# Performance work log

Measured on AMD Instinct MI355X. Metric: run time of the kernel, lower is better.

The kernel has to match this reference:

```python
import jax, jax.numpy as jnp
import numpy as np

B, N, D_IN, D_B, K = 32, 1024, 1024, 256, 16384


def setup_inputs() -> dict:
    key = jax.random.key(0)
    ks = jax.random.split(key, 8)
    s_in = 1.0 / np.sqrt(D_IN)
    s_b = 1.0 / np.sqrt(D_B)
    return {
        "x": jax.random.normal(ks[0], (B, N, D_IN), dtype=jnp.float32),
        "W_in": jax.random.uniform(ks[1], (D_IN, D_B), jnp.float32, -s_in, s_in),
        "b_in": jax.random.uniform(ks[2], (D_B,), jnp.float32, -s_in, s_in),
        "W_out": jax.random.uniform(ks[3], (D_B, D_IN), jnp.float32, -s_b, s_b),
        "b_out": jax.random.uniform(ks[4], (D_IN,), jnp.float32, -s_b, s_b),
        "codebook": jax.random.normal(ks[5], (K, D_B), dtype=jnp.float32),
        "W_proj": jax.random.uniform(ks[6], (D_B, D_B), jnp.float32, -s_b, s_b),
        "b_proj": jax.random.uniform(ks[7], (D_B,), jnp.float32, -s_b, s_b),
    }


def reference(x, W_in, b_in, W_out, b_out, codebook, W_proj, b_proj):
    # project_in
    z = jnp.einsum('bnd,de->bne', x, W_in) + b_in            # [B,N,Db]
    # SimVQ: projected codebook
    emb = codebook @ W_proj + b_proj                          # [K,Db]
    zf = z.reshape(-1, z.shape[-1])                           # [B*N,Db]
    # squared-distance argmin (cdist pattern)
    d = (jnp.sum(zf**2, axis=1, keepdims=True)
         + jnp.sum(emb**2, axis=1)
         - 2.0 * zf @ emb.T)                                  # [B*N,K]
    q_idx = jnp.argmin(d, axis=1)                             # [B*N]
    quantized = emb[q_idx].reshape(z.shape)                   # [B,N,Db]
    # straight-through
    reg_z = z + jax.lax.stop_gradient(quantized - z)
    # project_out
    x_hat = jnp.einsum('bnd,de->bne', reg_z, W_out) + b_out   # [B,N,Dout]
    bottleneck_rep = q_idx.reshape(z.shape[0], z.shape[1])
    return x_hat, bottleneck_rep, z, emb, reg_z
```

## Files before the change

### kernel.cpp

```cpp
#include <hip/hip_runtime.h>

typedef unsigned int u32;
typedef unsigned long long u64;
typedef unsigned short u16;

#define M_ROWS 32768
#define DB 256
#define DIN 1024
#define KCODES 16384

typedef __attribute__((ext_vector_type(8))) short bf16x8;
typedef __attribute__((ext_vector_type(4))) float f32x4;
typedef __attribute__((ext_vector_type(8))) unsigned short us8;

#define GLOAD16(gp, lp) __builtin_amdgcn_global_load_lds( \
    (const __attribute__((address_space(1))) unsigned int*)(gp), \
    (__attribute__((address_space(3))) unsigned int*)(lp), 16, 0, 0)

__device__ __forceinline__ u32 ford(float f) {
    u32 u = __float_as_uint(f);
    return (u & 0x80000000u) ? ~u : (u | 0x80000000u);
}
__device__ __forceinline__ u64 shfl_xor_u64(u64 v, int m) {
    u32 lo = (u32)v, hi = (u32)(v >> 32);
    lo = (u32)__shfl_xor((int)lo, m, 64);
    hi = (u32)__shfl_xor((int)hi, m, 64);
    return ((u64)hi << 32) | lo;
}
__device__ __forceinline__ u16 f2bf_rne(float f) {
    const u32 u = __float_as_uint(f);
    return (u16)((u + 0x7FFFu + ((u >> 16) & 1u)) >> 16);
}

__global__ __launch_bounds__(256)
void sgemm_f32(const float* __restrict__ A, int lda,
               const float* __restrict__ B, int ldb,
               const float* __restrict__ bias,
               float* __restrict__ C, int ldc, int Kd)
{
    __shared__ float As[16][132];
    __shared__ float Bs[16][132];
    const int t = threadIdx.x;
    const int w = t >> 6, lane = t & 63;
    const int tx = (lane & 7) | ((w & 1) << 3);
    const int ty = ((lane >> 3) & 7) | ((w >> 1) << 3);
    const int rb = blockIdx.x << 7;
    const int cb = blockIdx.y << 7;

    const int sr  = t >> 1;
    const int sk8 = (t & 1) << 3;
    const int bkr = t >> 4;
    const int bc8 = (t & 15) << 3;

    const float* Ap = A + (size_t)(rb + sr) * lda + sk8;
    const float* Bp = B + (size_t)bkr * ldb + cb + bc8;

    float acc[8][8];
#pragma unroll
    for (int i = 0; i < 8; ++i)
#pragma unroll
        for (int j = 0; j < 8; ++j) acc[i][j] = 0.0f;

    float4 a0 = *(const float4*)Ap;
    float4 a1 = *(const float4*)(Ap + 4);
    float4 b0 = *(const float4*)Bp;
    float4 b1 = *(const float4*)(Bp + 4);

    for (int kb = 0; kb < Kd; kb += 16) {
        __syncthreads();
        As[sk8 + 0][sr] = a0.x; As[sk8 + 1][sr] = a0.y;
        As[sk8 + 2][sr] = a0.z; As[sk8 + 3][sr] = a0.w;
        As[sk8 + 4][sr] = a1.x; As[sk8 + 5][sr] = a1.y;
        As[sk8 + 6][sr] = a1.z; As[sk8 + 7][sr] = a1.w;
        *(float4*)&Bs[bkr][bc8]     = b0;
        *(float4*)&Bs[bkr][bc8 + 4] = b1;
        __syncthreads();
        if (kb + 16 < Kd) {
            a0 = *(const float4*)(Ap + kb + 16);
            a1 = *(const float4*)(Ap + kb + 20);
            b0 = *(const float4*)(Bp + (size_t)(kb + 16) * ldb);
            b1 = *(const float4*)(Bp + (size_t)(kb + 16) * ldb + 4);
        }
#pragma unroll
        for (int kk = 0; kk < 16; ++kk) {
            float a[8], b[8];
            *(float4*)&a[0] = *(const float4*)&As[kk][ty * 8];
            *(float4*)&a[4] = *(const float4*)&As[kk][ty * 8 + 4];
            *(float4*)&b[0] = *(const float4*)&Bs[kk][tx * 8];
            *(float4*)&b[4] = *(const float4*)&Bs[kk][tx * 8 + 4];
#pragma unroll
            for (int i = 0; i < 8; ++i)
#pragma unroll
                for (int j = 0; j < 8; ++j)
                    acc[i][j] += a[i] * b[j];
        }
    }

    float bb[8];
#pragma unroll
    for (int j = 0; j < 8; ++j) bb[j] = bias[cb + tx * 8 + j];

#pragma unroll
    for (int i = 0; i < 8; ++i) {
        const size_t off = (size_t)(rb + ty * 8 + i) * ldc + cb + tx * 8;
        *(float4*)&C[off]     = make_float4(acc[i][0] + bb[0], acc[i][1] + bb[1],
                                            acc[i][2] + bb[2], acc[i][3] + bb[3]);
        *(float4*)&C[off + 4] = make_float4(acc[i][4] + bb[4], acc[i][5] + bb[5],
                                            acc[i][6] + bb[6], acc[i][7] + bb[7]);
    }
}

__global__ __launch_bounds__(256)
void split_pack(const float* __restrict__ X, u16* __restrict__ hi,
                u16* __restrict__ lo, float* __restrict__ s2)
{
    const int tid = (blockIdx.x << 8) + threadIdx.x;
    const int row = tid >> 5;
    const int kb  = (tid & 31) << 3;
    const float4 v0 = *(const float4*)(X + ((size_t)row << 8) + kb);
    const float4 v1 = *(const float4*)(X + ((size_t)row << 8) + kb + 4);
    const float f[8] = {v0.x, v0.y, v0.z, v0.w, v1.x, v1.y, v1.z, v1.w};
    us8 hv, lv;
    float s = 0.0f;
#pragma unroll
    for (int e = 0; e < 8; ++e) {
        const u16 h = f2bf_rne(f[e]);
        const float hf = __uint_as_float((u32)h << 16);
        hv[e] = h;
        lv[e] = f2bf_rne(f[e] - hf);
        s += f[e] * f[e];
    }
    const size_t off = ((size_t)(row >> 4) * 8 + (kb >> 5)) * 512
                     + (size_t)((kb >> 3) & 3) * 128 + ((row & 15) << 3);
    *(us8*)(hi + off) = hv;
    *(us8*)(lo + off) = lv;
#pragma unroll
    for (int m = 1; m <= 16; m <<= 1) s += __shfl_xor(s, m, 64);
    if ((threadIdx.x & 31) == 0) s2[row] = s;
}

__global__ __launch_bounds__(256)
void pack_wout(const float* __restrict__ W, u16* __restrict__ hi, u16* __restrict__ lo)
{
    const int tid = (blockIdx.x << 8) + threadIdx.x;
    const int n  = tid >> 5;
    const int kb = (tid & 31) << 3;
    us8 hv, lv;
#pragma unroll
    for (int e = 0; e < 8; ++e) {
        const float f = W[(size_t)(kb + e) * DIN + n];
        const u16 h = f2bf_rne(f);
        hv[e] = h;
        lv[e] = f2bf_rne(f - __uint_as_float((u32)h << 16));
    }
    const size_t off = ((size_t)(n >> 4) * 8 + (kb >> 5)) * 512
                     + (size_t)((kb >> 3) & 3) * 128 + ((n & 15) << 3);
    *(us8*)(hi + off) = hv;
    *(us8*)(lo + off) = lv;
}

__global__ __launch_bounds__(256)
void score_mfma(const u16* __restrict__ zh, const u16* __restrict__ zl,
                const u16* __restrict__ eh, const u16* __restrict__ el,
                const float* __restrict__ e2, u64* __restrict__ partial)
{
    __shared__ u16 smem[4][8][512];
    const int t = threadIdx.x;
    const int w = t >> 6, lane = t & 63;
    const int wr = w >> 1, wc = w & 1;
    const int rb = blockIdx.x << 7, cb = blockIdx.y << 7;
    const u32 lane8 = (u32)lane << 3;
    const int g = lane >> 4, li = lane & 15;

    const u32 zc0 = (u32)((rb >> 4) + w)     * 4096 + lane8;
    const u32 zc1 = (u32)((rb >> 4) + 4 + w) * 4096 + lane8;
    const u32 ec0 = (u32)((cb >> 4) + w)     * 4096 + lane8;
    const u32 ec1 = (u32)((cb >> 4) + 4 + w) * 4096 + lane8;

    u16* ZhL0 = &smem[0][w][0];      u16* ZhL1 = &smem[0][4 + w][0];
    u16* ZlL0 = &smem[1][w][0];      u16* ZlL1 = &smem[1][4 + w][0];
    u16* EhL0 = &smem[2][w][0];      u16* EhL1 = &smem[2][4 + w][0];
    u16* ElL0 = &smem[3][w][0];      u16* ElL1 = &smem[3][4 + w][0];

    int codes[4];
    float e2v[4];
#pragma unroll
    for (int j = 0; j < 4; ++j) {
        codes[j] = cb + wc * 64 + j * 16 + li;
        e2v[j] = e2[codes[j]];
    }

    f32x4 acc[4][4];
#pragma unroll
    for (int i = 0; i < 4; ++i)
#pragma unroll
        for (int j = 0; j < 4; ++j) {
            const float v = -0.5f * e2v[j];
            acc[i][j] = (f32x4){v, v, v, v};
        }

    for (int ks = 0; ks < 8; ++ks) {
        const u32 ko = (u32)ks << 9;
        if (ks) __syncthreads();
        GLOAD16(zh + zc0 + ko, ZhL0);  GLOAD16(zh + zc1 + ko, ZhL1);
        GLOAD16(zl + zc0 + ko, ZlL0);  GLOAD16(zl + zc1 + ko, ZlL1);
        GLOAD16(eh + ec0 + ko, EhL0);  GLOAD16(eh + ec1 + ko, EhL1);
        GLOAD16(el + ec0 + ko, ElL0);  GLOAD16(el + ec1 + ko, ElL1);
        __syncthreads();

        bf16x8 ah[4], al[4], bh[4], bl[4];
#pragma unroll
        for (int i = 0; i < 4; ++i) {
            ah[i] = *(const bf16x8*)&smem[0][wr * 4 + i][lane8];
            al[i] = *(const bf16x8*)&smem[1][wr * 4 + i][lane8];
            bh[i] = *(const bf16x8*)&smem[2][wc * 4 + i][lane8];
            bl[i] = *(const bf16x8*)&smem[3][wc * 4 + i][lane8];
        }
#pragma unroll
        for (int i = 0; i < 4; ++i)
#pragma unroll
            for (int j = 0; j < 4; ++j) {
                acc[i][j] = __builtin_amdgcn_mfma_f32_16x16x32_bf16(ah[i], bh[j], acc[i][j], 0, 0, 0);
                acc[i][j] = __builtin_amdgcn_mfma_f32_16x16x32_bf16(ah[i], bl[j], acc[i][j], 0, 0, 0);
                acc[i][j] = __builtin_amdgcn_mfma_f32_16x16x32_bf16(al[i], bh[j], acc[i][j], 0, 0, 0);
            }
    }

    const int slot = (blockIdx.y << 1) + wc;

#pragma unroll
    for (int i = 0; i < 4; ++i) {
#pragma unroll
        for (int r = 0; r < 4; ++r) {
            const int row = rb + wr * 64 + i * 16 + g * 4 + r;
            const float s0 = acc[i][0][r], s1 = acc[i][1][r];
            const float s2s = acc[i][2][r], s3 = acc[i][3][r];
            const float mm = fmaxf(fmaxf(s0, s1), fmaxf(s2s, s3));
            const u32 cj = (mm == s0) ? (u32)codes[0]
                         : (mm == s1) ? (u32)codes[1]
                         : (mm == s2s) ? (u32)codes[2] : (u32)codes[3];
            u64 key = ((u64)ford(-mm) << 32) | cj;
#pragma unroll
            for (int m = 1; m <= 8; m <<= 1) {
                const u64 o = shfl_xor_u64(key, m);
                key = (o < key) ? o : key;
            }
            if (li == 0) partial[((size_t)row << 8) + slot] = key;
        }
    }
}

__global__ __launch_bounds__(256)
void finalize2(const u64* __restrict__ partial, const float* __restrict__ Z,
               const float* __restrict__ E, const float* __restrict__ z2,
               const float* __restrict__ e2,
               float* __restrict__ bneck, float* __restrict__ regz,
               int* __restrict__ qidx)
{
    const int t = threadIdx.x;
    const int row = (blockIdx.x << 2) + (t >> 6);
    const int lane = t & 63;
    const u64* p = partial + ((size_t)row << 8);

    u64 a1 = ~0ull, a2 = ~0ull;
#pragma unroll
    for (int q = 0; q < 4; ++q) {
        const u64 k = p[(q << 6) + lane];
        if (k < a1) { a2 = a1; a1 = k; }
        else if (k < a2) { a2 = k; }
    }
#pragma unroll
    for (int m = 1; m <= 32; m <<= 1) {
        const u64 b1 = shfl_xor_u64(a1, m);
        const u64 b2 = shfl_xor_u64(a2, m);
        if (b1 < a1) { a2 = (a1 < b2) ? a1 : b2; a1 = b1; }
        else         { a2 = (a2 < b1) ? a2 : b1; }
    }
    const u32 i1 = (u32)a1 & (KCODES - 1);
    const u32 i2 = (u32)a2 & (KCODES - 1);

    const float4 zv  = *(const float4*)(Z + ((size_t)row << 8) + (lane << 2));
    const float4 c1v = *(const float4*)(E + ((size_t)i1 << 8) + (lane << 2));
    const float4 c2v = *(const float4*)(E + ((size_t)i2 << 8) + (lane << 2));
    float s1 = zv.x * c1v.x + zv.y * c1v.y + zv.z * c1v.z + zv.w * c1v.w;
    float s2 = zv.x * c2v.x + zv.y * c2v.y + zv.z * c2v.z + zv.w * c2v.w;
#pragma unroll
    for (int m = 32; m >= 1; m >>= 1) {
        s1 += __shfl_xor(s1, m, 64);
        s2 += __shfl_xor(s2, m, 64);
    }
    const float zz = z2[row];
    const float d1 = (zz + e2[i1]) - 2.0f * s1;
    const float d2 = (zz + e2[i2]) - 2.0f * s2;
    u32 win = i1;
    if (d2 < d1 || (d2 == d1 && i2 < i1)) win = i2;

    if (lane == 0) { qidx[row] = (int)win; bneck[row] = (float)win; }
    const float4 vw = *(const float4*)(E + ((size_t)win << 8) + (lane << 2));
    *(float4*)(regz + ((size_t)row << 8) + (lane << 2)) = vw;
}

__global__ __launch_bounds__(256)
void embout_mfma(const u16* __restrict__ ah_p, const u16* __restrict__ al_p,
                 const u16* __restrict__ bh_p, const u16* __restrict__ bl_p,
                 const float* __restrict__ bias, float* __restrict__ C)
{
    __shared__ u16 smem[4][8][512];
    const int t = threadIdx.x;
    const int w = t >> 6, lane = t & 63;
    const int wr = w >> 1, wc = w & 1;
    const int rb = blockIdx.x << 7, cb = blockIdx.y << 7;
    const u32 lane8 = (u32)lane << 3;
    const int g = lane >> 4, li = lane & 15;

    const u32 ac0 = (u32)((rb >> 4) + w)     * 4096 + lane8;
    const u32 ac1 = (u32)((rb >> 4) + 4 + w) * 4096 + lane8;
    const u32 bc0 = (u32)((cb >> 4) + w)     * 4096 + lane8;
    const u32 bc1 = (u32)((cb >> 4) + 4 + w) * 4096 + lane8;

    u16* AhL0 = &smem[0][w][0];      u16* AhL1 = &smem[0][4 + w][0];
    u16* AlL0 = &smem[1][w][0];      u16* AlL1 = &smem[1][4 + w][0];
    u16* BhL0 = &smem[2][w][0];      u16* BhL1 = &smem[2][4 + w][0];
    u16* BlL0 = &smem[3][w][0];      u16* BlL1 = &smem[3][4 + w][0];

    f32x4 acc[4][4];
#pragma unroll
    for (int i = 0; i < 4; ++i)
#pragma unroll
        for (int j = 0; j < 4; ++j) acc[i][j] = (f32x4){0.f, 0.f, 0.f, 0.f};

    for (int ks = 0; ks < 8; ++ks) {
        const u32 ko = (u32)ks << 9;
        if (ks) __syncthreads();
        GLOAD16(ah_p + ac0 + ko, AhL0);  GLOAD16(ah_p + ac1 + ko, AhL1);
        GLOAD16(al_p + ac0 + ko, AlL0);  GLOAD16(al_p + ac1 + ko, AlL1);
        GLOAD16(bh_p + bc0 + ko, BhL0);  GLOAD16(bh_p + bc1 + ko, BhL1);
        GLOAD16(bl_p + bc0 + ko, BlL0);  GLOAD16(bl_p + bc1 + ko, BlL1);
        __syncthreads();

        bf16x8 ah[4], al[4], bh[4], bl[4];
#pragma unroll
        for (int i = 0; i < 4; ++i) {
            ah[i] = *(const bf16x8*)&smem[0][wr * 4 + i][lane8];
            al[i] = *(const bf16x8*)&smem[1][wr * 4 + i][lane8];
            bh[i] = *(const bf16x8*)&smem[2][wc * 4 + i][lane8];
            bl[i] = *(const bf16x8*)&smem[3][wc * 4 + i][lane8];
        }
#pragma unroll
        for (int i = 0; i < 4; ++i)
#pragma unroll
            for (int j = 0; j < 4; ++j) {
                acc[i][j] = __builtin_amdgcn_mfma_f32_16x16x32_bf16(ah[i], bh[j], acc[i][j], 0, 0, 0);
                acc[i][j] = __builtin_amdgcn_mfma_f32_16x16x32_bf16(ah[i], bl[j], acc[i][j], 0, 0, 0);
                acc[i][j] = __builtin_amdgcn_mfma_f32_16x16x32_bf16(al[i], bh[j], acc[i][j], 0, 0, 0);
            }
    }

    float bv[4];
#pragma unroll
    for (int j = 0; j < 4; ++j) bv[j] = bias[cb + wc * 64 + j * 16 + li];

#pragma unroll
    for (int i = 0; i < 4; ++i)
#pragma unroll
        for (int j = 0; j < 4; ++j) {
            const int col = cb + wc * 64 + j * 16 + li;
#pragma unroll
            for (int r = 0; r < 4; ++r) {
                const int m = rb + wr * 64 + i * 16 + g * 4 + r;
                C[(size_t)m * DIN + col] = acc[i][j][r] + bv[j];
            }
        }
}

__global__ __launch_bounds__(256)
void gather_rows(const int* __restrict__ qidx, const float* __restrict__ S,
                 float* __restrict__ D)
{
    const int row = blockIdx.x;
    const int q = qidx[row] & (KCODES - 1);
    const float4 v = *(const float4*)(S + ((size_t)q << 10) + (threadIdx.x << 2));
    *(float4*)(D + ((size_t)row << 10) + (threadIdx.x << 2)) = v;
}

__global__ __launch_bounds__(256)
void xhat_gemm(const int* __restrict__ qidx, const float* __restrict__ E,
               const float* __restrict__ B, const float* __restrict__ bias,
               float* __restrict__ C)
{
    __shared__ float As[16][132];
    __shared__ float Bs[16][132];
    const int t = threadIdx.x;
    const int w = t >> 6, lane = t & 63;
    const int tx = (lane & 7) | ((w & 1) << 3);
    const int ty = ((lane >> 3) & 7) | ((w >> 1) << 3);
    const int rb = blockIdx.x << 7;
    const int cb = blockIdx.y << 7;

    const int sr  = t >> 1;
    const int sk8 = (t & 1) << 3;
    const int bkr = t >> 4;
    const int bc8 = (t & 15) << 3;

    const int aidx = qidx[rb + sr] & (KCODES - 1);
    const float* Ap = E + (size_t)aidx * DB + sk8;
    const float* Bp = B + (size_t)bkr * DIN + cb + bc8;

    float acc[8][8];
#pragma unroll
    for (int i = 0; i < 8; ++i)
#pragma unroll
        for (int j = 0; j < 8; ++j) acc[i][j] = 0.0f;

    float4 a0 = *(const float4*)Ap;
    float4 a1 = *(const float4*)(Ap + 4);
    float4 b0 = *(const float4*)Bp;
    float4 b1 = *(const float4*)(Bp + 4);

    for (int kb = 0; kb < DB; kb += 16) {
        __syncthreads();
        As[sk8 + 0][sr] = a0.x; As[sk8 + 1][sr] = a0.y;
        As[sk8 + 2][sr] = a0.z; As[sk8 + 3][sr] = a0.w;
        As[sk8 + 4][sr] = a1.x; As[sk8 + 5][sr] = a1.y;
        As[sk8 + 6][sr] = a1.z; As[sk8 + 7][sr] = a1.w;
        *(float4*)&Bs[bkr][bc8]     = b0;
        *(float4*)&Bs[bkr][bc8 + 4] = b1;
        __syncthreads();
        if (kb + 16 < DB) {
            a0 = *(const float4*)(Ap + kb + 16);
            a1 = *(const float4*)(Ap + kb + 20);
            b0 = *(const float4*)(Bp + (size_t)(kb + 16) * DIN);
            b1 = *(const float4*)(Bp + (size_t)(kb + 16) * DIN + 4);
        }
#pragma unroll
        for (int kk = 0; kk < 16; ++kk) {
            float a[8], b[8];
            *(float4*)&a[0] = *(const float4*)&As[kk][ty * 8];
            *(float4*)&a[4] = *(const float4*)&As[kk][ty * 8 + 4];
            *(float4*)&b[0] = *(const float4*)&Bs[kk][tx * 8];
            *(float4*)&b[4] = *(const float4*)&Bs[kk][tx * 8 + 4];
#pragma unroll
            for (int i = 0; i < 8; ++i)
#pragma unroll
                for (int j = 0; j < 8; ++j)
                    acc[i][j] += a[i] * b[j];
        }
    }

    float bb[8];
#pragma unroll
    for (int j = 0; j < 8; ++j) bb[j] = bias[cb + tx * 8 + j];

#pragma unroll
    for (int i = 0; i < 8; ++i) {
        const size_t off = (size_t)(rb + ty * 8 + i) * DIN + cb + tx * 8;
        *(float4*)&C[off]     = make_float4(acc[i][0] + bb[0], acc[i][1] + bb[1],
                                            acc[i][2] + bb[2], acc[i][3] + bb[3]);
        *(float4*)&C[off + 4] = make_float4(acc[i][4] + bb[4], acc[i][5] + bb[5],
                                            acc[i][6] + bb[6], acc[i][7] + bb[7]);
    }
}

extern "C" void kernel_launch(void* const* d_in, const int* in_sizes, int n_in,
                              void* d_out, int out_size, void* d_ws, size_t ws_size,
                              hipStream_t stream)
{
    const float* x        = (const float*)d_in[0];
    const float* W_in     = (const float*)d_in[1];
    const float* b_in     = (const float*)d_in[2];
    const float* W_out    = (const float*)d_in[3];
    const float* b_out    = (const float*)d_in[4];
    const float* codebook = (const float*)d_in[5];
    const float* W_proj   = (const float*)d_in[6];
    const float* b_proj   = (const float*)d_in[7];

    float* out   = (float*)d_out;
    float* xhat  = out;
    float* bneck = out + 33554432;
    float* z     = out + 33587200;
    float* emb   = out + 41975808;
    float* regz  = out + 46170112;

    char* outc = (char*)d_out;
    u64* partial = (u64*)outc;
    u16* eh = (u16*)(outc + 67108864);
    u16* el = (u16*)(outc + 75497472);
    u16* zh = (u16*)(outc + 184680448);
    u16* zl = (u16*)(outc + 201457664);

    char* ws = (char*)d_ws;
    float* e2   = (float*)ws;
    float* z2   = (float*)(ws + 65536);
    int*   qidx = (int*)  (ws + 196608);
    u16*   whh     = (u16*)  (ws + 327680);
    u16*   whl     = (u16*)  (ws + 851968);
    float* emb_out = (float*)(ws + 1376256);
    const bool fast_xhat = (ws_size >= (size_t)1376256 + 67108864);

    sgemm_f32<<<dim3(128, 2), 256, 0, stream>>>(codebook, DB, W_proj, DB, b_proj,
                                                emb, DB, DB);
    split_pack<<<KCODES / 8, 256, 0, stream>>>(emb, eh, el, e2);
    if (fast_xhat) {
        pack_wout<<<DIN / 8, 256, 0, stream>>>(W_out, whh, whl);
        embout_mfma<<<dim3(KCODES / 128, DIN / 128), 256, 0, stream>>>(
            eh, el, whh, whl, b_out, emb_out);
    }
    sgemm_f32<<<dim3(256, 2), 256, 0, stream>>>(x, DIN, W_in, DB, b_in,
                                                z, DB, DIN);
    split_pack<<<M_ROWS / 8, 256, 0, stream>>>(z, zh, zl, z2);
    score_mfma<<<dim3(M_ROWS / 128, KCODES / 128), 256, 0, stream>>>(
        zh, zl, eh, el, e2, partial);
    finalize2<<<M_ROWS / 4, 256, 0, stream>>>(partial, z, emb, z2, e2,
                                              bneck, regz, qidx);
    if (fast_xhat) {
        gather_rows<<<M_ROWS, 256, 0, stream>>>(qidx, emb_out, xhat);
    } else {
        xhat_gemm<<<dim3(256, 8), 256, 0, stream>>>(qidx, emb, W_out, b_out, xhat);
    }
}
```

Measured before the change: 1.411 ms.

## Double-buffer LDS tiles in score and output-projection MFMA kernels

```diff
diff --git a/kernel.cpp b/kernel.cpp
--- a/kernel.cpp
+++ b/kernel.cpp
@@ -164,7 +164,7 @@
                 const u16* __restrict__ eh, const u16* __restrict__ el,
                 const float* __restrict__ e2, u64* __restrict__ partial)
 {
-    __shared__ u16 smem[4][8][512];
+    __shared__ u16 smem[2][4][8][512];
     const int t = threadIdx.x;
     const int w = t >> 6, lane = t & 63;
     const int wr = w >> 1, wc = w & 1;
@@ -177,11 +177,6 @@
     const u32 ec0 = (u32)((cb >> 4) + w)     * 4096 + lane8;
     const u32 ec1 = (u32)((cb >> 4) + 4 + w) * 4096 + lane8;
 
-    u16* ZhL0 = &smem[0][w][0];      u16* ZhL1 = &smem[0][4 + w][0];
-    u16* ZlL0 = &smem[1][w][0];      u16* ZlL1 = &smem[1][4 + w][0];
-    u16* EhL0 = &smem[2][w][0];      u16* EhL1 = &smem[2][4 + w][0];
-    u16* ElL0 = &smem[3][w][0];      u16* ElL1 = &smem[3][4 + w][0];
-
     int codes[4];
     float e2v[4];
 #pragma unroll
@@ -199,22 +194,30 @@
             acc[i][j] = (f32x4){v, v, v, v};
         }
 
+    GLOAD16(zh + zc0, &smem[0][0][w][0]);  GLOAD16(zh + zc1, &smem[0][0][4 + w][0]);
+    GLOAD16(zl + zc0, &smem[0][1][w][0]);  GLOAD16(zl + zc1, &smem[0][1][4 + w][0]);
+    GLOAD16(eh + ec0, &smem[0][2][w][0]);  GLOAD16(eh + ec1, &smem[0][2][4 + w][0]);
+    GLOAD16(el + ec0, &smem[0][3][w][0]);  GLOAD16(el + ec1, &smem[0][3][4 + w][0]);
+
+    int b = 0;
     for (int ks = 0; ks < 8; ++ks) {
-        const u32 ko = (u32)ks << 9;
-        if (ks) __syncthreads();
-        GLOAD16(zh + zc0 + ko, ZhL0);  GLOAD16(zh + zc1 + ko, ZhL1);
-        GLOAD16(zl + zc0 + ko, ZlL0);  GLOAD16(zl + zc1 + ko, ZlL1);
-        GLOAD16(eh + ec0 + ko, EhL0);  GLOAD16(eh + ec1 + ko, EhL1);
-        GLOAD16(el + ec0 + ko, ElL0);  GLOAD16(el + ec1 + ko, ElL1);
         __syncthreads();
+        if (ks < 7) {
+            const u32 ko = (u32)(ks + 1) << 9;
+            const int nb = b ^ 1;
+            GLOAD16(zh + zc0 + ko, &smem[nb][0][w][0]);  GLOAD16(zh + zc1 + ko, &smem[nb][0][4 + w][0]);
+            GLOAD16(zl + zc0 + ko, &smem[nb][1][w][0]);  GLOAD16(zl + zc1 + ko, &smem[nb][1][4 + w][0]);
+            GLOAD16(eh + ec0 + ko, &smem[nb][2][w][0]);  GLOAD16(eh + ec1 + ko, &smem[nb][2][4 + w][0]);
+            GLOAD16(el + ec0 + ko, &smem[nb][3][w][0]);  GLOAD16(el + ec1 + ko, &smem[nb][3][4 + w][0]);
+        }
 
         bf16x8 ah[4], al[4], bh[4], bl[4];
 #pragma unroll
         for (int i = 0; i < 4; ++i) {
-            ah[i] = *(const bf16x8*)&smem[0][wr * 4 + i][lane8];
-            al[i] = *(const bf16x8*)&smem[1][wr * 4 + i][lane8];
-            bh[i] = *(const bf16x8*)&smem[2][wc * 4 + i][lane8];
-            bl[i] = *(const bf16x8*)&smem[3][wc * 4 + i][lane8];
+            ah[i] = *(const bf16x8*)&smem[b][0][wr * 4 + i][lane8];
+            al[i] = *(const bf16x8*)&smem[b][1][wr * 4 + i][lane8];
+            bh[i] = *(const bf16x8*)&smem[b][2][wc * 4 + i][lane8];
+            bl[i] = *(const bf16x8*)&smem[b][3][wc * 4 + i][lane8];
         }
 #pragma unroll
         for (int i = 0; i < 4; ++i)
@@ -224,6 +227,7 @@
                 acc[i][j] = __builtin_amdgcn_mfma_f32_16x16x32_bf16(ah[i], bl[j], acc[i][j], 0, 0, 0);
                 acc[i][j] = __builtin_amdgcn_mfma_f32_16x16x32_bf16(al[i], bh[j], acc[i][j], 0, 0, 0);
             }
+        b ^= 1;
     }
 
     const int slot = (blockIdx.y << 1) + wc;
@@ -305,7 +309,7 @@
                  const u16* __restrict__ bh_p, const u16* __restrict__ bl_p,
                  const float* __restrict__ bias, float* __restrict__ C)
 {
-    __shared__ u16 smem[4][8][512];
+    __shared__ u16 smem[2][4][8][512];
     const int t = threadIdx.x;
     const int w = t >> 6, lane = t & 63;
     const int wr = w >> 1, wc = w & 1;
@@ -318,33 +322,36 @@
     const u32 bc0 = (u32)((cb >> 4) + w)     * 4096 + lane8;
     const u32 bc1 = (u32)((cb >> 4) + 4 + w) * 4096 + lane8;
 
-    u16* AhL0 = &smem[0][w][0];      u16* AhL1 = &smem[0][4 + w][0];
-    u16* AlL0 = &smem[1][w][0];      u16* AlL1 = &smem[1][4 + w][0];
-    u16* BhL0 = &smem[2][w][0];      u16* BhL1 = &smem[2][4 + w][0];
-    u16* BlL0 = &smem[3][w][0];      u16* BlL1 = &smem[3][4 + w][0];
-
     f32x4 acc[4][4];
 #pragma unroll
     for (int i = 0; i < 4; ++i)
 #pragma unroll
         for (int j = 0; j < 4; ++j) acc[i][j] = (f32x4){0.f, 0.f, 0.f, 0.f};
 
+    GLOAD16(ah_p + ac0, &smem[0][0][w][0]);  GLOAD16(ah_p + ac1, &smem[0][0][4 + w][0]);
+    GLOAD16(al_p + ac0, &smem[0][1][w][0]);  GLOAD16(al_p + ac1, &smem[0][1][4 + w][0]);
+    GLOAD16(bh_p + bc0, &smem[0][2][w][0]);  GLOAD16(bh_p + bc1, &smem[0][2][4 + w][0]);
+    GLOAD16(bl_p + bc0, &smem[0][3][w][0]);  GLOAD16(bl_p + bc1, &smem[0][3][4 + w][0]);
+
+    int b = 0;
     for (int ks = 0; ks < 8; ++ks) {
-        const u32 ko = (u32)ks << 9;
-        if (ks) __syncthreads();
-        GLOAD16(ah_p + ac0 + ko, AhL0);  GLOAD16(ah_p + ac1 + ko, AhL1);
-        GLOAD16(al_p + ac0 + ko, AlL0);  GLOAD16(al_p + ac1 + ko, AlL1);
-        GLOAD16(bh_p + bc0 + ko, BhL0);  GLOAD16(bh_p + bc1 + ko, BhL1);
-        GLOAD16(bl_p + bc0 + ko, BlL0);  GLOAD16(bl_p + bc1 + ko, BlL1);
         __syncthreads();
+        if (ks < 7) {
+            const u32 ko = (u32)(ks + 1) << 9;
+            const int nb = b ^ 1;
+            GLOAD16(ah_p + ac0 + ko, &smem[nb][0][w][0]);  GLOAD16(ah_p + ac1 + ko, &smem[nb][0][4 + w][0]);
+            GLOAD16(al_p + ac0 + ko, &smem[nb][1][w][0]);  GLOAD16(al_p + ac1 + ko, &smem[nb][1][4 + w][0]);
+            GLOAD16(bh_p + bc0 + ko, &smem[nb][2][w][0]);  GLOAD16(bh_p + bc1 + ko, &smem[nb][2][4 + w][0]);
+            GLOAD16(bl_p + bc0 + ko, &smem[nb][3][w][0]);  GLOAD16(bl_p + bc1 + ko, &smem[nb][3][4 + w][0]);
+        }
 
         bf16x8 ah[4], al[4], bh[4], bl[4];
 #pragma unroll
         for (int i = 0; i < 4; ++i) {
-            ah[i] = *(const bf16x8*)&smem[0][wr * 4 + i][lane8];
-            al[i] = *(const bf16x8*)&smem[1][wr * 4 + i][lane8];
-            bh[i] = *(const bf16x8*)&smem[2][wc * 4 + i][lane8];
-            bl[i] = *(const bf16x8*)&smem[3][wc * 4 + i][lane8];
+            ah[i] = *(const bf16x8*)&smem[b][0][wr * 4 + i][lane8];
+            al[i] = *(const bf16x8*)&smem[b][1][wr * 4 + i][lane8];
+            bh[i] = *(const bf16x8*)&smem[b][2][wc * 4 + i][lane8];
+            bl[i] = *(const bf16x8*)&smem[b][3][wc * 4 + i][lane8];
         }
 #pragma unroll
         for (int i = 0; i < 4; ++i)
@@ -354,6 +361,7 @@
                 acc[i][j] = __builtin_amdgcn_mfma_f32_16x16x32_bf16(ah[i], bl[j], acc[i][j], 0, 0, 0);
                 acc[i][j] = __builtin_amdgcn_mfma_f32_16x16x32_bf16(al[i], bh[j], acc[i][j], 0, 0, 0);
             }
+        b ^= 1;
     }
 
     float bv[4];
```

Result: slower. 1.469 ms (+4.1%).

## Double-buffer LDS tiles in score kernel to overlap loads with MFMA

Applied to the files above, without the earlier changes.

```diff
diff --git a/kernel.cpp b/kernel.cpp
--- a/kernel.cpp
+++ b/kernel.cpp
@@ -164,7 +164,7 @@
                 const u16* __restrict__ eh, const u16* __restrict__ el,
                 const float* __restrict__ e2, u64* __restrict__ partial)
 {
-    __shared__ u16 smem[4][8][512];
+    __shared__ u16 smem[2][4][8][512];
     const int t = threadIdx.x;
     const int w = t >> 6, lane = t & 63;
     const int wr = w >> 1, wc = w & 1;
@@ -177,11 +177,6 @@
     const u32 ec0 = (u32)((cb >> 4) + w)     * 4096 + lane8;
     const u32 ec1 = (u32)((cb >> 4) + 4 + w) * 4096 + lane8;
 
-    u16* ZhL0 = &smem[0][w][0];      u16* ZhL1 = &smem[0][4 + w][0];
-    u16* ZlL0 = &smem[1][w][0];      u16* ZlL1 = &smem[1][4 + w][0];
-    u16* EhL0 = &smem[2][w][0];      u16* EhL1 = &smem[2][4 + w][0];
-    u16* ElL0 = &smem[3][w][0];      u16* ElL1 = &smem[3][4 + w][0];
-
     int codes[4];
     float e2v[4];
 #pragma unroll
@@ -199,22 +194,36 @@
             acc[i][j] = (f32x4){v, v, v, v};
         }
 
+#define STAGE(B, KO) do { \
+    GLOAD16(zh + zc0 + (KO), &smem[B][0][w][0]);  GLOAD16(zh + zc1 + (KO), &smem[B][0][4 + w][0]); \
+    GLOAD16(zl + zc0 + (KO), &smem[B][1][w][0]);  GLOAD16(zl + zc1 + (KO), &smem[B][1][4 + w][0]); \
+    GLOAD16(eh + ec0 + (KO), &smem[B][2][w][0]);  GLOAD16(eh + ec1 + (KO), &smem[B][2][4 + w][0]); \
+    GLOAD16(el + ec0 + (KO), &smem[B][3][w][0]);  GLOAD16(el + ec1 + (KO), &smem[B][3][4 + w][0]); \
+} while (0)
+
+    asm volatile("s_waitcnt vmcnt(0)" ::: "memory");
+    __builtin_amdgcn_sched_barrier(0);
+
+    STAGE(0, 0u);
+    STAGE(1, 512u);
+
+#pragma unroll
     for (int ks = 0; ks < 8; ++ks) {
-        const u32 ko = (u32)ks << 9;
-        if (ks) __syncthreads();
-        GLOAD16(zh + zc0 + ko, ZhL0);  GLOAD16(zh + zc1 + ko, ZhL1);
-        GLOAD16(zl + zc0 + ko, ZlL0);  GLOAD16(zl + zc1 + ko, ZlL1);
-        GLOAD16(eh + ec0 + ko, EhL0);  GLOAD16(eh + ec1 + ko, EhL1);
-        GLOAD16(el + ec0 + ko, ElL0);  GLOAD16(el + ec1 + ko, ElL1);
-        __syncthreads();
-
+        if (ks < 7) { asm volatile("s_waitcnt vmcnt(8)" ::: "memory"); }
+        else        { asm volatile("s_waitcnt vmcnt(0)" ::: "memory"); }
+        __builtin_amdgcn_sched_barrier(0);
+        __builtin_amdgcn_s_barrier();
+        asm volatile("" ::: "memory");
+        __builtin_amdgcn_sched_barrier(0);
+
+        const int b = ks & 1;
         bf16x8 ah[4], al[4], bh[4], bl[4];
 #pragma unroll
         for (int i = 0; i < 4; ++i) {
-            ah[i] = *(const bf16x8*)&smem[0][wr * 4 + i][lane8];
-            al[i] = *(const bf16x8*)&smem[1][wr * 4 + i][lane8];
-            bh[i] = *(const bf16x8*)&smem[2][wc * 4 + i][lane8];
-            bl[i] = *(const bf16x8*)&smem[3][wc * 4 + i][lane8];
+            ah[i] = *(const bf16x8*)&smem[b][0][wr * 4 + i][lane8];
+            al[i] = *(const bf16x8*)&smem[b][1][wr * 4 + i][lane8];
+            bh[i] = *(const bf16x8*)&smem[b][2][wc * 4 + i][lane8];
+            bl[i] = *(const bf16x8*)&smem[b][3][wc * 4 + i][lane8];
         }
 #pragma unroll
         for (int i = 0; i < 4; ++i)
@@ -224,7 +233,15 @@
                 acc[i][j] = __builtin_amdgcn_mfma_f32_16x16x32_bf16(ah[i], bl[j], acc[i][j], 0, 0, 0);
                 acc[i][j] = __builtin_amdgcn_mfma_f32_16x16x32_bf16(al[i], bh[j], acc[i][j], 0, 0, 0);
             }
-    }
+
+        __builtin_amdgcn_sched_barrier(0);
+        asm volatile("" ::: "memory");
+        __builtin_amdgcn_s_barrier();
+        asm volatile("" ::: "memory");
+        __builtin_amdgcn_sched_barrier(0);
+        if (ks < 6) STAGE(b, (u32)(ks + 2) << 9);
+    }
+#undef STAGE
 
     const int slot = (blockIdx.y << 1) + wc;
 
```

New measurement: 1.433 ms. No clear change (+1.6%).

## Fuse z projection with bf16 hi/lo packing and pre-reduce score partials in-block

Applied to the files above, without the earlier changes.

```diff
diff --git a/kernel.cpp b/kernel.cpp
--- a/kernel.cpp
+++ b/kernel.cpp
@@ -111,6 +111,109 @@
 }
 
 __global__ __launch_bounds__(256)
+void sgemm_z_pack(const float* __restrict__ A, const float* __restrict__ B,
+                  const float* __restrict__ bias, float* __restrict__ C,
+                  u16* __restrict__ zh, u16* __restrict__ zl)
+{
+    __shared__ float As[16][132];
+    __shared__ float Bs[16][132];
+    const int t = threadIdx.x;
+    const int w = t >> 6, lane = t & 63;
+    const int tx = (lane & 7) | ((w & 1) << 3);
+    const int ty = ((lane >> 3) & 7) | ((w >> 1) << 3);
+    const int rb = blockIdx.x << 7;
+    const int cb = blockIdx.y << 7;
+
+    const int sr  = t >> 1;
+    const int sk8 = (t & 1) << 3;
+    const int bkr = t >> 4;
+    const int bc8 = (t & 15) << 3;
+
+    const float* Ap = A + (size_t)(rb + sr) * DIN + sk8;
+    const float* Bp = B + (size_t)bkr * DB + cb + bc8;
+
+    float acc[8][8];
+#pragma unroll
+    for (int i = 0; i < 8; ++i)
+#pragma unroll
+        for (int j = 0; j < 8; ++j) acc[i][j] = 0.0f;
+
+    float4 a0 = *(const float4*)Ap;
+    float4 a1 = *(const float4*)(Ap + 4);
+    float4 b0 = *(const float4*)Bp;
+    float4 b1 = *(const float4*)(Bp + 4);
+
+    for (int kb = 0; kb < DIN; kb += 16) {
+        __syncthreads();
+        As[sk8 + 0][sr] = a0.x; As[sk8 + 1][sr] = a0.y;
+        As[sk8 + 2][sr] = a0.z; As[sk8 + 3][sr] = a0.w;
+        As[sk8 + 4][sr] = a1.x; As[sk8 + 5][sr] = a1.y;
+        As[sk8 + 6][sr] = a1.z; As[sk8 + 7][sr] = a1.w;
+        *(float4*)&Bs[bkr][bc8]     = b0;
+        *(float4*)&Bs[bkr][bc8 + 4] = b1;
+        __syncthreads();
+        if (kb + 16 < DIN) {
+            a0 = *(const float4*)(Ap + kb + 16);
+            a1 = *(const float4*)(Ap + kb + 20);
+            b0 = *(const float4*)(Bp + (size_t)(kb + 16) * DB);
+            b1 = *(const float4*)(Bp + (size_t)(kb + 16) * DB + 4);
+        }
+#pragma unroll
+        for (int kk = 0; kk < 16; ++kk) {
+            float a[8], b[8];
+            *(float4*)&a[0] = *(const float4*)&As[kk][ty * 8];
+            *(float4*)&a[4] = *(const float4*)&As[kk][ty * 8 + 4];
+            *(float4*)&b[0] = *(const float4*)&Bs[kk][tx * 8];
+            *(float4*)&b[4] = *(const float4*)&Bs[kk][tx * 8 + 4];
+#pragma unroll
+            for (int i = 0; i < 8; ++i)
+#pragma unroll
+                for (int j = 0; j < 8; ++j)
+                    acc[i][j] += a[i] * b[j];
+        }
+    }
+
+    float bb[8];
+#pragma unroll
+    for (int j = 0; j < 8; ++j) bb[j] = bias[cb + tx * 8 + j];
+
+#pragma unroll
+    for (int i = 0; i < 8; ++i) {
+        const int rg = rb + ty * 8 + i;
+        float zr[8];
+#pragma unroll
+        for (int j = 0; j < 8; ++j) zr[j] = acc[i][j] + bb[j];
+        const size_t off = (size_t)rg * DB + cb + tx * 8;
+        *(float4*)&C[off]     = make_float4(zr[0], zr[1], zr[2], zr[3]);
+        *(float4*)&C[off + 4] = make_float4(zr[4], zr[5], zr[6], zr[7]);
+        us8 hv, lv;
+#pragma unroll
+        for (int j = 0; j < 8; ++j) {
+            const u16 h = f2bf_rne(zr[j]);
+            hv[j] = h;
+            lv[j] = f2bf_rne(zr[j] - __uint_as_float((u32)h << 16));
+        }
+        const size_t poff = ((size_t)(rg >> 4) * 8 + (size_t)(cb >> 5) + (tx >> 2)) * 512
+                          + (size_t)(tx & 3) * 128 + ((rg & 15) << 3);
+        *(us8*)(zh + poff) = hv;
+        *(us8*)(zl + poff) = lv;
+    }
+}
+
+__global__ __launch_bounds__(256)
+void rowsq_kernel(const float* __restrict__ X, float* __restrict__ s2)
+{
+    const int t = threadIdx.x;
+    const int row = (blockIdx.x << 2) + (t >> 6);
+    const int lane = t & 63;
+    const float4 v = *(const float4*)(X + (size_t)row * DB + (lane << 2));
+    float s = v.x * v.x + v.y * v.y + v.z * v.z + v.w * v.w;
+#pragma unroll
+    for (int m = 32; m >= 1; m >>= 1) s += __shfl_xor(s, m, 64);
+    if (lane == 0) s2[row] = s;
+}
+
+__global__ __launch_bounds__(256)
 void split_pack(const float* __restrict__ X, u16* __restrict__ hi,
                 u16* __restrict__ lo, float* __restrict__ s2)
 {
@@ -165,6 +268,7 @@
                 const float* __restrict__ e2, u64* __restrict__ partial)
 {
     __shared__ u16 smem[4][8][512];
+    __shared__ u64 lkeys[2][2][64];
     const int t = threadIdx.x;
     const int w = t >> 6, lane = t & 63;
     const int wr = w >> 1, wc = w & 1;
@@ -226,13 +330,10 @@
             }
     }
 
-    const int slot = (blockIdx.y << 1) + wc;
-
 #pragma unroll
     for (int i = 0; i < 4; ++i) {
 #pragma unroll
         for (int r = 0; r < 4; ++r) {
-            const int row = rb + wr * 64 + i * 16 + g * 4 + r;
             const float s0 = acc[i][0][r], s1 = acc[i][1][r];
             const float s2s = acc[i][2][r], s3 = acc[i][3][r];
             const float mm = fmaxf(fmaxf(s0, s1), fmaxf(s2s, s3));
@@ -245,8 +346,15 @@
                 const u64 o = shfl_xor_u64(key, m);
                 key = (o < key) ? o : key;
             }
-            if (li == 0) partial[((size_t)row << 8) + slot] = key;
-        }
+            if (li == 0) lkeys[wc][wr][i * 16 + g * 4 + r] = key;
+        }
+    }
+    __syncthreads();
+    if (wc == 0) {
+        const u64 m0 = lkeys[0][wr][lane];
+        const u64 m1 = lkeys[1][wr][lane];
+        const u64 mk = (m0 < m1) ? m0 : m1;
+        partial[((size_t)(rb + wr * 64 + lane) << 7) + blockIdx.y] = mk;
     }
 }
 
@@ -260,15 +368,12 @@
     const int t = threadIdx.x;
     const int row = (blockIdx.x << 2) + (t >> 6);
     const int lane = t & 63;
-    const u64* p = partial + ((size_t)row << 8);
-
-    u64 a1 = ~0ull, a2 = ~0ull;
-#pragma unroll
-    for (int q = 0; q < 4; ++q) {
-        const u64 k = p[(q << 6) + lane];
-        if (k < a1) { a2 = a1; a1 = k; }
-        else if (k < a2) { a2 = k; }
-    }
+    const u64* p = partial + ((size_t)row << 7);
+
+    const u64 k0 = p[lane];
+    const u64 k1 = p[64 + lane];
+    u64 a1 = (k0 < k1) ? k0 : k1;
+    u64 a2 = (k0 < k1) ? k1 : k0;
 #pragma unroll
     for (int m = 1; m <= 32; m <<= 1) {
         const u64 b1 = shfl_xor_u64(a1, m);
@@ -505,9 +610,8 @@
         embout_mfma<<<dim3(KCODES / 128, DIN / 128), 256, 0, stream>>>(
             eh, el, whh, whl, b_out, emb_out);
     }
-    sgemm_f32<<<dim3(256, 2), 256, 0, stream>>>(x, DIN, W_in, DB, b_in,
-                                                z, DB, DIN);
-    split_pack<<<M_ROWS / 8, 256, 0, stream>>>(z, zh, zl, z2);
+    sgemm_z_pack<<<dim3(256, 2), 256, 0, stream>>>(x, W_in, b_in, z, zh, zl);
+    rowsq_kernel<<<M_ROWS / 4, 256, 0, stream>>>(z, z2);
     score_mfma<<<dim3(M_ROWS / 128, KCODES / 128), 256, 0, stream>>>(
         zh, zl, eh, el, e2, partial);
     finalize2<<<M_ROWS / 4, 256, 0, stream>>>(partial, z, emb, z2, e2,
```

After: 1.371 ms. 1.03x faster.
